# Kernel optimization log

Measured on AMD Instinct MI355X. Metric: run time of the kernel, lower is better.

Reference implementation:

```python
import jax, jax.numpy as jnp
import numpy as np

MAX_ITERS = 20


def setup_inputs() -> dict:
    key = jax.random.key(0)
    k1, k2 = jax.random.split(key)
    bs, n_y, n_x, n_t, f = 16, 64, 64, 32, 4
    # coarse water depths (non-negative)
    u_coarse = jax.random.uniform(k1, (bs, n_y, n_x, n_t), dtype=jnp.float32) * 2.0
    # fine topography patch [n_y*f, n_x*f]
    topo = jax.random.normal(k2, (n_y * f, n_x * f), dtype=jnp.float32)
    return {"u_coarse": u_coarse, "topo": topo}


def reference(u_coarse, topo):
    bs, n_y, n_x, n_t = u_coarse.shape
    f = topo.shape[0] // n_y
    # fold fine topo into per-coarse-cell patches: [n_y, n_x, f*f]
    z = topo.reshape(n_y, f, n_x, f).transpose(0, 2, 1, 3).reshape(n_y, n_x, f * f)
    z_fine = z[None, :, :, None, :]                      # [1, n_y, n_x, 1, f*f]
    d_target = u_coarse[..., None]                       # [bs, n_y, n_x, n_t, 1]

    h_low = jnp.broadcast_to(jnp.min(z_fine, axis=-1, keepdims=True), d_target.shape)
    h_high = jnp.max(z_fine, axis=-1, keepdims=True) + d_target + 0.001

    # fixed-trip-count bisection on water surface elevation per (cell, t)
    for _ in range(MAX_ITERS):
        h_mid = (h_low + h_high) * 0.5
        d_mid = jnp.mean(jax.nn.relu(h_mid - z_fine), axis=-1, keepdims=True)
        mask = d_mid < d_target
        h_low = jnp.where(mask, h_mid, h_low)
        h_high = jnp.where(mask, h_high, h_mid)

    h_final = (h_low + h_high) * 0.5
    u_rec = jax.nn.relu(h_final - z_fine)                # [bs, n_y, n_x, n_t, f*f]
    u_rec = u_rec.reshape(bs, n_y, n_x, n_t, f, f)
    u_rec = u_rec.transpose(0, 1, 4, 2, 5, 3).reshape(bs, n_y * f, n_x * f, n_t)
    return u_rec
```

## Files before the change

kernel.cpp:

```cpp
#include <hip/hip_runtime.h>


__global__ __launch_bounds__(256) void bathtub_kernel(
    const float* __restrict__ u_coarse,
    const float* __restrict__ topo,
    float* __restrict__ out,
    int total)
{
    const int idx = blockIdx.x * 256 + threadIdx.x;
    if (idx >= total) return;

    const int t    = idx & 31;
    const int cell = idx >> 5;
    const int x    = cell & 63;
    const int y    = (cell >> 6) & 63;
    const int b    = cell >> 12;

    float z[16];
    const float* trow = topo + (y * 4) * 256 + x * 4;
#pragma unroll
    for (int fy = 0; fy < 4; ++fy) {
        const float4 v = *reinterpret_cast<const float4*>(trow + fy * 256);
        z[fy * 4 + 0] = v.x;
        z[fy * 4 + 1] = v.y;
        z[fy * 4 + 2] = v.z;
        z[fy * 4 + 3] = v.w;
    }

    const float d = u_coarse[idx];

    float s[16];
#pragma unroll
    for (int k = 0; k < 16; ++k) s[k] = z[k];

#pragma unroll
    for (int k = 2; k <= 16; k <<= 1) {
#pragma unroll
        for (int j = k >> 1; j > 0; j >>= 1) {
#pragma unroll
            for (int i = 0; i < 16; ++i) {
                const int ixj = i ^ j;
                if (ixj > i) {
                    const bool asc = ((i & k) == 0);
                    const float a = s[i], c = s[ixj];
                    const float lo = fminf(a, c), hi = fmaxf(a, c);
                    s[i]   = asc ? lo : hi;
                    s[ixj] = asc ? hi : lo;
                }
            }
        }
    }

    float S[16];
    float run = 0.0f;
#pragma unroll
    for (int k = 0; k < 16; ++k) { run += s[k]; S[k] = run; }

    const float T16 = 16.0f * d;
    float h = (T16 + S[15]) * (1.0f / 16.0f);
#pragma unroll
    for (int j = 15; j >= 1; --j) {
        const float hj = (T16 + S[j - 1]) * (1.0f / (float)j);
        h = (hj <= s[j]) ? hj : h;
    }

    const int obase = ((b * 256 + y * 4) * 256 + x * 4) * 32 + t;
#pragma unroll
    for (int fy = 0; fy < 4; ++fy) {
#pragma unroll
        for (int fx = 0; fx < 4; ++fx) {
            out[obase + (fy * 256 + fx) * 32] = fmaxf(h - z[fy * 4 + fx], 0.0f);
        }
    }
}

extern "C" void kernel_launch(void* const* d_in, const int* in_sizes, int n_in,
                              void* d_out, int out_size, void* d_ws, size_t ws_size,
                              hipStream_t stream) {
    const float* u_coarse = (const float*)d_in[0];
    const float* topo     = (const float*)d_in[1];
    float* out            = (float*)d_out;

    const int total  = in_sizes[0];
    const int blocks = (total + 255) / 256;
    bathtub_kernel<<<blocks, 256, 0, stream>>>(u_coarse, topo, out, total);
}
```

Measured before the change: 27.78 us.

## Process four time steps per thread with float4 loads and stores

Each thread now handles four consecutive time steps of one coarse cell. The topography patch is loaded once, sorted once and prefix-summed once, then reused for all four steps instead of being redone per step. Input depths are read and outputs written as float4 vectors. This cuts redundant sorting and load work and widens memory transactions, in exchange for four times fewer threads and somewhat more registers per thread.

```diff
diff --git a/kernel.cpp b/kernel.cpp
--- a/kernel.cpp
+++ b/kernel.cpp
@@ -5,13 +5,13 @@
     const float* __restrict__ u_coarse,
     const float* __restrict__ topo,
     float* __restrict__ out,
-    int total)
+    int nquads)
 {
-    const int idx = blockIdx.x * 256 + threadIdx.x;
-    if (idx >= total) return;
+    const int tid = blockIdx.x * 256 + threadIdx.x;
+    if (tid >= nquads) return;
 
-    const int t    = idx & 31;
-    const int cell = idx >> 5;
+    const int tq   = tid & 7;
+    const int cell = tid >> 3;
     const int x    = cell & 63;
     const int y    = (cell >> 6) & 63;
     const int b    = cell >> 12;
@@ -27,7 +27,8 @@
         z[fy * 4 + 3] = v.w;
     }
 
-    const float d = u_coarse[idx];
+    const float4 d4 = *reinterpret_cast<const float4*>(u_coarse + tid * 4);
+    float dd[4] = {d4.x, d4.y, d4.z, d4.w};
 
     float s[16];
 #pragma unroll
@@ -56,20 +57,31 @@
 #pragma unroll
     for (int k = 0; k < 16; ++k) { run += s[k]; S[k] = run; }
 
-    const float T16 = 16.0f * d;
-    float h = (T16 + S[15]) * (1.0f / 16.0f);
+    float h[4];
 #pragma unroll
-    for (int j = 15; j >= 1; --j) {
-        const float hj = (T16 + S[j - 1]) * (1.0f / (float)j);
-        h = (hj <= s[j]) ? hj : h;
+    for (int i = 0; i < 4; ++i) {
+        const float T16 = 16.0f * dd[i];
+        float hv = (T16 + S[15]) * (1.0f / 16.0f);
+#pragma unroll
+        for (int j = 15; j >= 1; --j) {
+            const float hj = (T16 + S[j - 1]) * (1.0f / (float)j);
+            hv = (hj <= s[j]) ? hj : hv;
+        }
+        h[i] = hv;
     }
 
-    const int obase = ((b * 256 + y * 4) * 256 + x * 4) * 32 + t;
+    const int obase = ((b * 256 + y * 4) * 256 + x * 4) * 32 + tq * 4;
 #pragma unroll
     for (int fy = 0; fy < 4; ++fy) {
 #pragma unroll
         for (int fx = 0; fx < 4; ++fx) {
-            out[obase + (fy * 256 + fx) * 32] = fmaxf(h - z[fy * 4 + fx], 0.0f);
+            const float zz = z[fy * 4 + fx];
+            float4 v;
+            v.x = fmaxf(h[0] - zz, 0.0f);
+            v.y = fmaxf(h[1] - zz, 0.0f);
+            v.z = fmaxf(h[2] - zz, 0.0f);
+            v.w = fmaxf(h[3] - zz, 0.0f);
+            *reinterpret_cast<float4*>(out + obase + (fy * 256 + fx) * 32) = v;
         }
     }
 }
@@ -81,7 +93,7 @@
     const float* topo     = (const float*)d_in[1];
     float* out            = (float*)d_out;
 
-    const int total  = in_sizes[0];
-    const int blocks = (total + 255) / 256;
-    bathtub_kernel<<<blocks, 256, 0, stream>>>(u_coarse, topo, out, total);
+    const int nquads = in_sizes[0] / 4;
+    const int blocks = (nquads + 255) / 256;
+    bathtub_kernel<<<blocks, 256, 0, stream>>>(u_coarse, topo, out, nquads);
 }
```

Measured after the change: 27.50 us, median of 2. About the same (-1.0%).
